# Kernel tuning notes

Measured on AMD Instinct MI355X. Metric: run time of the kernel, lower is better.

The kernel has to match this reference:

```python
import jax, jax.numpy as jnp
import numpy as np

B, T, D, E, C = 2, 2048, 2048, 8, 512
O1 = D // E  # per-expert hidden width (out_features // num_experts)


def setup_inputs() -> dict:
    key = jax.random.key(0)
    k = jax.random.split(key, 8)
    s = 1.0 / np.sqrt(D)
    return {
        "x": jax.random.normal(k[0], (B, T, D), dtype=jnp.float32),
        "dispatch_mask": jax.random.uniform(k[1], (B, T, E, C), dtype=jnp.float32),
        "combine_array": jax.random.uniform(k[2], (B, T, E, C), dtype=jnp.float32),
        # contract weights: nn.Linear(D, D) reshaped to (E, D//E, D)
        "W1": jax.random.uniform(k[3], (E, O1, D), jnp.float32, -s, s),
        "b1": jax.random.uniform(k[4], (E, O1), jnp.float32, -s, s),
        # expand weights: nn.Linear(D, D) reshaped to (E, D, D//E)
        "W2": jax.random.uniform(k[5], (E, D, O1), jnp.float32, -s, s),
        "b2": jax.random.uniform(k[6], (D,), jnp.float32, -s, s),
    }


def reference(x, dispatch_mask, combine_array, W1, b1, W2, b2):
    # --- ExpertsChooseMaskedContract ---
    # einsum('btd,btec,eod->beco') split into two GEMM-shaped contractions
    xe = jnp.einsum('btd,btec->becd', x, dispatch_mask)          # [B,E,C,D]
    h = jnp.einsum('becd,eod->beco', xe, W1) + b1[None, :, None, :]  # [B,E,C,O1]
    # --- GELU (torch nn.GELU default = exact erf form) ---
    h = jax.nn.gelu(h, approximate=False)
    # --- ExpertsChooseMaskedExpand (homogeneous-coords bias == add b2 then combine) ---
    y = jnp.einsum('beci,eoi->beco', h, W2) + b2[None, None, None, :]  # [B,E,C,D]
    out = jnp.einsum('beco,btec->bto', y, combine_array)          # [B,T,D]
    return out
```

## Files before the change

### kernel.cpp

```cpp
#include <hip/hip_runtime.h>
#include <math.h>

#define BB 2
#define TT 2048
#define DD 2048
#define EE 8
#define CCv 512
#define OO1 256

typedef unsigned short u16;
typedef __bf16 bf16x8 __attribute__((ext_vector_type(8)));
typedef float f32x4 __attribute__((ext_vector_type(4)));

__device__ __forceinline__ u16 f2bf(float f) {
    unsigned u = __float_as_uint(f);
    unsigned r = (u + 0x7fffu + ((u >> 16) & 1u)) >> 16;
    return (u16)r;
}

__device__ __forceinline__ void gload16(const void* g, void* s) {
    __builtin_amdgcn_global_load_lds(
        (const __attribute__((address_space(1))) void*)g,
        (__attribute__((address_space(3))) void*)s, 16, 0, 0);
}

__global__ __launch_bounds__(256) void conv_cast(const float* __restrict__ in,
                                                 u16* __restrict__ out, long n) {
    long i = ((long)blockIdx.x * 256 + threadIdx.x) * 4;
    float4 v = *(const float4*)&in[i];
    ushort4 o; o.x = f2bf(v.x); o.y = f2bf(v.y); o.z = f2bf(v.z); o.w = f2bf(v.w);
    *(ushort4*)&out[i] = o;
}

__global__ __launch_bounds__(256) void transpose_conv(
    const float* __restrict__ in, long inHi, long inLo, int modZ, long sIn,
    u16* __restrict__ out, long outZ, long sOut)
{
    __shared__ float tile[32][33];
    const int z = blockIdx.z;
    const float* ib = in + (long)(z / modZ) * inHi + (long)(z % modZ) * inLo;
    u16* ob = out + (long)z * outZ;
    const int t0 = blockIdx.y * 32, c0 = blockIdx.x * 32;
    const int tid = threadIdx.x;
    const int r = tid >> 3, c4 = (tid & 7) * 4;

    float4 v = *(const float4*)&ib[(long)(t0 + r) * sIn + c0 + c4];
    tile[r][c4 + 0] = v.x; tile[r][c4 + 1] = v.y;
    tile[r][c4 + 2] = v.z; tile[r][c4 + 3] = v.w;
    __syncthreads();

    const int oc = tid >> 3, t4 = (tid & 7) * 4;
    ushort4 o;
    o.x = f2bf(tile[t4 + 0][oc]);
    o.y = f2bf(tile[t4 + 1][oc]);
    o.z = f2bf(tile[t4 + 2][oc]);
    o.w = f2bf(tile[t4 + 3][oc]);
    *(ushort4*)&ob[(long)(c0 + oc) * sOut + t0 + t4] = o;
}

template<int EPI>
__global__ __launch_bounds__(256)
void mfma_gemm(const u16* __restrict__ A, long ldA, long aHi, long aLo, int modA,
               const u16* __restrict__ B, long ldB, long bHi, long bLo, int modB,
               void* __restrict__ Cout, long ldC, long cHi, long cLo, int modC,
               const float* __restrict__ bias, long biasLo, int modBias,
               int M, int N, int K)
{
    __shared__ __align__(16) char smem[32768];
    char* smA = smem;
    char* smB = smem + 16384;

    const int z = blockIdx.z;
    const char* Ab = (const char*)(A + (long)(z / modA) * aHi + (long)(z % modA) * aLo);
    const char* Bb = (const char*)(B + (long)(z / modB) * bHi + (long)(z % modB) * bLo);
    const long ldAb = ldA * 2, ldBb = ldB * 2;

    const int m0 = blockIdx.y * 128, n0 = blockIdx.x * 128;
    const int tid = threadIdx.x;
    const int l = tid & 63;
    const int w = tid >> 6;
    const int wm = w >> 1, wn = w & 1;

    const int srow = l >> 3;
    const int schunk = (l & 7) ^ srow;
    const int frow = l & 15;
    const int fgrp = l >> 4;
    const int fch0 = fgrp ^ (l & 7);

    int aoff[4], boff[4];
#pragma unroll
    for (int i = 0; i < 4; ++i) {
        aoff[i] = (wm * 64 + i * 16 + frow) * 128 + fch0 * 16;
        boff[i] = (wn * 64 + i * 16 + frow) * 128 + fch0 * 16;
    }

    f32x4 acc[4][4];
    const f32x4 zero4 = {0.f, 0.f, 0.f, 0.f};
#pragma unroll
    for (int i = 0; i < 4; ++i)
#pragma unroll
        for (int j = 0; j < 4; ++j) acc[i][j] = zero4;

    const long sgo = (long)schunk * 16;

    for (int k0 = 0; k0 < K; k0 += 64) {
        const long kb = (long)k0 * 2;
#pragma unroll
        for (int j = 0; j < 4; ++j) {
            const int rr = (j * 4 + w) * 8 + srow;
            gload16(Ab + (long)(m0 + rr) * ldAb + kb + sgo, smA + (j * 4 + w) * 1024);
            gload16(Bb + (long)(n0 + rr) * ldBb + kb + sgo, smB + (j * 4 + w) * 1024);
        }
        __syncthreads();
#pragma unroll
        for (int kk = 0; kk < 2; ++kk) {
            const int kx = kk * 64;
            bf16x8 af[4], bfr[4];
#pragma unroll
            for (int i = 0; i < 4; ++i) af[i] = *(const bf16x8*)(smA + (aoff[i] ^ kx));
#pragma unroll
            for (int i = 0; i < 4; ++i) bfr[i] = *(const bf16x8*)(smB + (boff[i] ^ kx));
#pragma unroll
            for (int mi = 0; mi < 4; ++mi)
#pragma unroll
                for (int ni = 0; ni < 4; ++ni)
                    acc[mi][ni] = __builtin_amdgcn_mfma_f32_16x16x32_bf16(
                        af[mi], bfr[ni], acc[mi][ni], 0, 0, 0);
        }
        __syncthreads();
    }

    const long cbase = (long)(z / modC) * cHi + (long)(z % modC) * cLo;
    const float* biasB = bias + (long)(z % modBias) * biasLo;
#pragma unroll
    for (int mi = 0; mi < 4; ++mi) {
#pragma unroll
        for (int ni = 0; ni < 4; ++ni) {
            const int col = n0 + wn * 64 + ni * 16 + frow;
            const int rowb = m0 + wm * 64 + mi * 16 + fgrp * 4;
#pragma unroll
            for (int r = 0; r < 4; ++r) {
                float v = acc[mi][ni][r];
                const int row = rowb + r;
                if (EPI == 1) {
                    v += biasB[col];
                    v = 0.5f * v * (1.0f + erff(v * 0.70710678118654752f));
                } else {
                    v += biasB[row];
                }
                ((u16*)Cout)[cbase + (long)row * ldC + col] = f2bf(v);
            }
        }
    }
}

template<int OUTBF>
__global__ __launch_bounds__(512, 2)
void mfma_gemm_big(const u16* __restrict__ A, long ldA, long aHi, long aLo, int modA,
                   const u16* __restrict__ B, long ldB, long bHi, long bLo, int modB,
                   void* __restrict__ Cout, long ldC, long cHi, long cLo, int modC,
                   int M, int N, int K)
{
    __shared__ __align__(16) char smem[147456];

    const int z = blockIdx.z;
    const char* Ab = (const char*)(A + (long)(z / modA) * aHi + (long)(z % modA) * aLo);
    const char* Bb = (const char*)(B + (long)(z / modB) * bHi + (long)(z % modB) * bLo);
    const long ldAb = ldA * 2, ldBb = ldB * 2;

    const int m0 = blockIdx.y * 256, n0 = blockIdx.x * 128;
    const int tid = threadIdx.x;
    const int l = tid & 63;
    const int w = tid >> 6;
    const int wm = w >> 2, wn = w & 3;

    const int srow = l >> 3;
    const int schunk = (l & 7) ^ srow;
    const long sgo = (long)schunk * 16;
    const int frow = l & 15;
    const int fgrp = l >> 4;
    const int fsw = (fgrp ^ (l & 7)) * 16;

    auto stageA = [&](int kt, int bsel, int j) {
        const int rr = (j * 8 + w) * 8 + srow;
        gload16(Ab + (long)(m0 + rr) * ldAb + (long)kt * 128 + sgo,
                smem + bsel * 49152 + (j * 8 + w) * 1024);
    };
    auto stageB = [&](int kt, int bsel, int j) {
        const int rr = (j * 8 + w) * 8 + srow;
        gload16(Bb + (long)(n0 + rr) * ldBb + (long)kt * 128 + sgo,
                smem + bsel * 49152 + 32768 + (j * 8 + w) * 1024);
    };

    f32x4 acc[8][2];
    const f32x4 zero4 = {0.f, 0.f, 0.f, 0.f};
#pragma unroll
    for (int i = 0; i < 8; ++i) { acc[i][0] = zero4; acc[i][1] = zero4; }

#pragma unroll
    for (int j = 0; j < 4; ++j) stageA(0, 0, j);
#pragma unroll
    for (int j = 0; j < 2; ++j) stageB(0, 0, j);
#pragma unroll
    for (int j = 0; j < 4; ++j) stageA(1, 1, j);
#pragma unroll
    for (int j = 0; j < 2; ++j) stageB(1, 1, j);
    asm volatile("s_waitcnt vmcnt(6)" ::: "memory");
    __builtin_amdgcn_s_barrier();

    const int NT = K >> 6;
    int bc = 0;
    int sc = 2;
    for (int kt = 0; kt < NT; ++kt) {
        const char* bufA = smem + bc * 49152;
        const char* bufB = bufA + 32768;
        const bool pf = (kt + 2) < NT;
        const int kpf = kt + 2;
        bf16x8 af[4][2];
#pragma unroll
        for (int p = 0; p < 4; ++p) {
            const int qm = p >> 1, qn = p & 1;
            if (qn == 0) {
#pragma unroll
                for (int mi = 0; mi < 4; ++mi) {
                    const int ab = (wm * 128 + (qm * 4 + mi) * 16 + frow) * 128 + fsw;
                    af[mi][0] = *(const bf16x8*)(bufA + ab);
                    af[mi][1] = *(const bf16x8*)(bufA + (ab ^ 64));
                }
            }
            bf16x8 bfr[2];
            const int bb0 = (wn * 32 + qn * 16 + frow) * 128 + fsw;
            bfr[0] = *(const bf16x8*)(bufB + bb0);
            bfr[1] = *(const bf16x8*)(bufB + (bb0 ^ 64));
            if (pf) {
                if (p == 0)      { stageA(kpf, sc, 0); stageA(kpf, sc, 1); }
                else if (p == 1) { stageA(kpf, sc, 2); stageA(kpf, sc, 3); }
                else if (p == 2) { stageB(kpf, sc, 0); }
                else             { stageB(kpf, sc, 1); }
            }
            __builtin_amdgcn_s_barrier();
            asm volatile("s_waitcnt lgkmcnt(0)" ::: "memory");
            __builtin_amdgcn_s_setprio(1);
#pragma unroll
            for (int mi = 0; mi < 4; ++mi) {
                acc[qm * 4 + mi][qn] = __builtin_amdgcn_mfma_f32_16x16x32_bf16(
                    af[mi][0], bfr[0], acc[qm * 4 + mi][qn], 0, 0, 0);
                acc[qm * 4 + mi][qn] = __builtin_amdgcn_mfma_f32_16x16x32_bf16(
                    af[mi][1], bfr[1], acc[qm * 4 + mi][qn], 0, 0, 0);
            }
            __builtin_amdgcn_s_setprio(0);
            __builtin_amdgcn_s_barrier();
        }
        if (pf) { asm volatile("s_waitcnt vmcnt(6)" ::: "memory"); }
        else    { asm volatile("s_waitcnt vmcnt(0)" ::: "memory"); }
        __builtin_amdgcn_s_barrier();
        bc = (bc == 2) ? 0 : bc + 1;
        sc = (sc == 2) ? 0 : sc + 1;
    }

    const long cbase = (long)(z / modC) * cHi + (long)(z % modC) * cLo;
#pragma unroll
    for (int Mi = 0; Mi < 8; ++Mi) {
#pragma unroll
        for (int ni = 0; ni < 2; ++ni) {
            const int col = n0 + wn * 32 + ni * 16 + frow;
            const int rowb = m0 + wm * 128 + Mi * 16 + fgrp * 4;
#pragma unroll
            for (int r = 0; r < 4; ++r) {
                const float v = acc[Mi][ni][r];
                const long idx = cbase + (long)(rowb + r) * ldC + col;
                if (OUTBF) ((u16*)Cout)[idx] = f2bf(v);
                else       ((float*)Cout)[idx] = v;
            }
        }
    }
}

extern "C" void kernel_launch(void* const* d_in, const int* in_sizes, int n_in,
                              void* d_out, int out_size, void* d_ws, size_t ws_size,
                              hipStream_t stream) {
    const float* x    = (const float*)d_in[0];
    const float* mask = (const float*)d_in[1];
    const float* comb = (const float*)d_in[2];
    const float* W1   = (const float*)d_in[3];
    const float* b1   = (const float*)d_in[4];
    const float* W2   = (const float*)d_in[5];
    const float* b2   = (const float*)d_in[6];
    float* out = (float*)d_out;

    char* ws = (char*)d_ws;
    u16* buf0 = (u16*)ws;
    u16* xT   = (u16*)(ws + 33554432);
    u16* W1b  = (u16*)(ws + 50331648);
    u16* W2b  = (u16*)(ws + 58720256);
    u16* xe   = (u16*)(ws + 67108864);
    u16* h    = (u16*)(ws + 100663296);
    u16* yT   = xe;

    transpose_conv<<<dim3(DD / 32, TT / 32, BB), 256, 0, stream>>>(
        x, (long)TT * DD, 0L, 1, (long)DD, xT, (long)DD * TT, (long)TT);
    transpose_conv<<<dim3(CCv / 32, TT / 32, BB * EE), 256, 0, stream>>>(
        mask, (long)TT * EE * CCv, (long)CCv, EE, (long)EE * CCv,
        buf0, (long)CCv * TT, (long)TT);
    conv_cast<<<(int)((8L * OO1 * DD) / 1024), 256, 0, stream>>>(W1, W1b, 8L * OO1 * DD);
    conv_cast<<<(int)((8L * DD * OO1) / 1024), 256, 0, stream>>>(W2, W2b, 8L * DD * OO1);

    mfma_gemm_big<1><<<dim3(DD / 128, CCv / 256, 16), 512, 0, stream>>>(
        buf0, 2048, 1048576L, 0L, 1,
        xT,   2048, 4194304L, 0L, 8,
        xe,   2048, 1048576L, 0L, 1,
        CCv, DD, TT);

    conv_cast<<<(int)((2L * TT * EE * CCv) / 1024), 256, 0, stream>>>(
        comb, buf0, 2L * TT * EE * CCv);

    mfma_gemm<1><<<dim3(OO1 / 128, CCv / 128, 16), 256, 0, stream>>>(
        xe,  2048, 1048576L, 0L, 1,
        W1b, 2048, 0L, 524288L, 8,
        h,   256, 131072L, 0L, 1,
        b1, 256L, 8, CCv, OO1, DD);

    mfma_gemm<3><<<dim3(CCv / 128, DD / 128, 16), 256, 0, stream>>>(
        W2b, 256, 0L, 524288L, 8,
        h,   256, 131072L, 0L, 1,
        yT,  4096, 8388608L, 512L, 8,
        b2, 0L, 1, DD, CCv, OO1);

    mfma_gemm_big<0><<<dim3(DD / 128, TT / 256, BB), 512, 0, stream>>>(
        buf0, 4096, 8388608L, 0L, 1,
        yT,   4096, 8388608L, 0L, 1,
        out,  2048, 4194304L, 0L, 1,
        TT, DD, EE * CCv);
}
```

Measured before the change: 302.7 us.

## Retile GEMM waves to 64x64 and simplify k-loop into single load-then-MFMA phase

Changes the warp layout in the big MFMA GEMM from 2x4 waves with 128x32 tiles to 4x2 waves with 64x64 tiles. Each wave now loads 4 A and 4 B fragments per k-step, giving a more square register tile with better LDS reuse per fragment. The four-phase interleaved schedule, with its prefetch spread and per-phase barriers, is replaced by one prefetch burst, one fragment load and 32 back-to-back MFMAs per k-tile. This removes many barriers, but the LDS reads now overlap less with the MFMAs.

```diff
diff --git a/kernel.cpp b/kernel.cpp
--- a/kernel.cpp
+++ b/kernel.cpp
@@ -172,7 +172,7 @@
     const int tid = threadIdx.x;
     const int l = tid & 63;
     const int w = tid >> 6;
-    const int wm = w >> 2, wn = w & 3;
+    const int wm = w >> 1, wn = w & 1;
 
     const int srow = l >> 3;
     const int schunk = (l & 7) ^ srow;
@@ -192,10 +192,12 @@
                 smem + bsel * 49152 + 32768 + (j * 8 + w) * 1024);
     };
 
-    f32x4 acc[8][2];
+    f32x4 acc[4][4];
     const f32x4 zero4 = {0.f, 0.f, 0.f, 0.f};
 #pragma unroll
-    for (int i = 0; i < 8; ++i) { acc[i][0] = zero4; acc[i][1] = zero4; }
+    for (int i = 0; i < 4; ++i)
+#pragma unroll
+        for (int j = 0; j < 4; ++j) acc[i][j] = zero4;
 
 #pragma unroll
     for (int j = 0; j < 4; ++j) stageA(0, 0, j);
@@ -215,59 +217,57 @@
         const char* bufA = smem + bc * 49152;
         const char* bufB = bufA + 32768;
         const bool pf = (kt + 2) < NT;
-        const int kpf = kt + 2;
-        bf16x8 af[4][2];
-#pragma unroll
-        for (int p = 0; p < 4; ++p) {
-            const int qm = p >> 1, qn = p & 1;
-            if (qn == 0) {
-#pragma unroll
-                for (int mi = 0; mi < 4; ++mi) {
-                    const int ab = (wm * 128 + (qm * 4 + mi) * 16 + frow) * 128 + fsw;
-                    af[mi][0] = *(const bf16x8*)(bufA + ab);
-                    af[mi][1] = *(const bf16x8*)(bufA + (ab ^ 64));
-                }
-            }
-            bf16x8 bfr[2];
-            const int bb0 = (wn * 32 + qn * 16 + frow) * 128 + fsw;
-            bfr[0] = *(const bf16x8*)(bufB + bb0);
-            bfr[1] = *(const bf16x8*)(bufB + (bb0 ^ 64));
-            if (pf) {
-                if (p == 0)      { stageA(kpf, sc, 0); stageA(kpf, sc, 1); }
-                else if (p == 1) { stageA(kpf, sc, 2); stageA(kpf, sc, 3); }
-                else if (p == 2) { stageB(kpf, sc, 0); }
-                else             { stageB(kpf, sc, 1); }
-            }
-            __builtin_amdgcn_s_barrier();
-            asm volatile("s_waitcnt lgkmcnt(0)" ::: "memory");
-            __builtin_amdgcn_s_setprio(1);
-#pragma unroll
-            for (int mi = 0; mi < 4; ++mi) {
-                acc[qm * 4 + mi][qn] = __builtin_amdgcn_mfma_f32_16x16x32_bf16(
-                    af[mi][0], bfr[0], acc[qm * 4 + mi][qn], 0, 0, 0);
-                acc[qm * 4 + mi][qn] = __builtin_amdgcn_mfma_f32_16x16x32_bf16(
-                    af[mi][1], bfr[1], acc[qm * 4 + mi][qn], 0, 0, 0);
-            }
-            __builtin_amdgcn_s_setprio(0);
-            __builtin_amdgcn_s_barrier();
-        }
+
+        if (pf) {
+            const int kpf = kt + 2;
+            stageA(kpf, sc, 0); stageA(kpf, sc, 1);
+            stageA(kpf, sc, 2); stageA(kpf, sc, 3);
+            stageB(kpf, sc, 0); stageB(kpf, sc, 1);
+        }
+
+        bf16x8 af[4][2], bfr[4][2];
+#pragma unroll
+        for (int mi = 0; mi < 4; ++mi) {
+            const int ab = (wm * 64 + mi * 16 + frow) * 128 + fsw;
+            af[mi][0] = *(const bf16x8*)(bufA + ab);
+            af[mi][1] = *(const bf16x8*)(bufA + (ab ^ 64));
+        }
+#pragma unroll
+        for (int ni = 0; ni < 4; ++ni) {
+            const int bb = (wn * 64 + ni * 16 + frow) * 128 + fsw;
+            bfr[ni][0] = *(const bf16x8*)(bufB + bb);
+            bfr[ni][1] = *(const bf16x8*)(bufB + (bb ^ 64));
+        }
+
+        __builtin_amdgcn_s_setprio(1);
+#pragma unroll
+        for (int kk = 0; kk < 2; ++kk)
+#pragma unroll
+            for (int mi = 0; mi < 4; ++mi)
+#pragma unroll
+                for (int ni = 0; ni < 4; ++ni)
+                    acc[mi][ni] = __builtin_amdgcn_mfma_f32_16x16x32_bf16(
+                        af[mi][kk], bfr[ni][kk], acc[mi][ni], 0, 0, 0);
+        __builtin_amdgcn_s_setprio(0);
+
         if (pf) { asm volatile("s_waitcnt vmcnt(6)" ::: "memory"); }
         else    { asm volatile("s_waitcnt vmcnt(0)" ::: "memory"); }
         __builtin_amdgcn_s_barrier();
+
         bc = (bc == 2) ? 0 : bc + 1;
         sc = (sc == 2) ? 0 : sc + 1;
     }
 
     const long cbase = (long)(z / modC) * cHi + (long)(z % modC) * cLo;
 #pragma unroll
-    for (int Mi = 0; Mi < 8; ++Mi) {
-#pragma unroll
-        for (int ni = 0; ni < 2; ++ni) {
-            const int col = n0 + wn * 32 + ni * 16 + frow;
-            const int rowb = m0 + wm * 128 + Mi * 16 + fgrp * 4;
+    for (int mi = 0; mi < 4; ++mi) {
+#pragma unroll
+        for (int ni = 0; ni < 4; ++ni) {
+            const int col = n0 + wn * 64 + ni * 16 + frow;
+            const int rowb = m0 + wm * 64 + mi * 16 + fgrp * 4;
 #pragma unroll
             for (int r = 0; r < 4; ++r) {
-                const float v = acc[Mi][ni][r];
+                const float v = acc[mi][ni][r];
                 const long idx = cbase + (long)(rowb + r) * ldC + col;
                 if (OUTBF) ((u16*)Cout)[idx] = f2bf(v);
                 else       ((float*)Cout)[idx] = v;
```

Measured after the change: 277.2 us. 1.09x faster.
